# Kernel optimization log

Measured on AMD Instinct MI355X. Metric: run time of the kernel, lower is better.

Reference implementation:

```python
import jax, jax.numpy as jnp
import numpy as np

SR = 2  # sr_ratio

def _avgpool2x2(x):
    # x: [B,C,H,W] -> [B,C,H//2,W//2]
    B, C, H, W = x.shape
    return x.reshape(B, C, H // SR, SR, W // SR, SR).mean(axis=(3, 5))

def setup_inputs() -> dict:
    key = jax.random.key(0)
    ks = jax.random.split(key, 6)
    B, C, H, W = 8, 256, 64, 64
    d = C // 8
    sc_qk = 1.0 / np.sqrt(C)
    return {
        "x": jax.random.normal(ks[0], (B, C, H, W), jnp.float32),
        "wq": jax.random.normal(ks[1], (d, C), jnp.float32) * sc_qk,
        "wk": jax.random.normal(ks[2], (d, C), jnp.float32) * sc_qk,
        "wv": jax.random.normal(ks[3], (C, C), jnp.float32) * sc_qk,
        "wo": jax.random.normal(ks[4], (C, C), jnp.float32) * sc_qk,
        "gamma": jax.random.normal(ks[5], (1,), jnp.float32),
    }

def reference(x, wq, wk, wv, wo, gamma):
    B, C, H, W = x.shape
    N = H * W
    d = wq.shape[0]
    # q: conv1x1 then flatten+transpose -> [B, N, d]
    q = jnp.einsum('dc,bchw->bhwd', wq, x).reshape(B, N, d)
    # spatial reduction of K/V source
    x_kv = _avgpool2x2(x)
    Hk, Wk = x_kv.shape[2], x_kv.shape[3]
    Nk = Hk * Wk
    k = jnp.einsum('dc,bchw->bdhw', wk, x_kv).reshape(B, d, Nk)   # [B,d,Nk]
    v = jnp.einsum('oc,bchw->bohw', wv, x_kv).reshape(B, C, Nk)   # [B,C,Nk]
    # attn = softmax(q @ k / sqrt(d)) over Nk
    attn = jax.nn.softmax(jnp.einsum('bnd,bdm->bnm', q, k) / jnp.sqrt(jnp.float32(d)), axis=-1)
    # out = v @ attn^T -> [B,C,N]
    out = jnp.einsum('bcm,bnm->bcn', v, attn).reshape(B, C, H, W)
    out = jnp.einsum('oc,bchw->bohw', wo, out)
    return x + gamma[0] * out
```

## Files before the change

### kernel.cpp

```cpp
#include <hip/hip_runtime.h>

#define BB 8
#define CC 256
#define NN 4096
#define DD 32
#define NK 1024

typedef unsigned short u16;
typedef unsigned int   u32;
typedef __attribute__((ext_vector_type(8))) short bf16x8;
typedef __attribute__((ext_vector_type(4))) float f32x4;

#define MFMA16 __builtin_amdgcn_mfma_f32_16x16x32_bf16

#define OFF_WVO  0u
#define OFF_WQB  32768u
#define OFF_WKB  36864u
#define OFF_QF   40960u
#define OFF_KF   565248u
#define OFF_VOF  696320u

__device__ __forceinline__ u16 f2bf(float f) {
    u32 u = __float_as_uint(f);
    u += 0x7FFFu + ((u >> 16) & 1u);
    return (u16)(u >> 16);
}

__device__ __forceinline__ u32 cvt_pk_bf16(float lo, float hi) {
    u32 r;
    asm("v_cvt_pk_bf16_f32 %0, %1, %2" : "=v"(r) : "v"(lo), "v"(hi));
    return r;
}

__launch_bounds__(1024)
__global__ void wprep_kernel(const float* __restrict__ wq, const float* __restrict__ wk,
                             const float* __restrict__ wv, const float* __restrict__ wo,
                             u16* __restrict__ wqb, u16* __restrict__ wkb,
                             u16* __restrict__ wvob) {
    __shared__ float part[4][256];
    int o = blockIdx.x, t = threadIdx.x;
    int jq = t >> 8, c = t & 255;
    const float* wvp = wv + (size_t)(jq * 64) * CC + c;
    const float* wop = wo + o * CC + jq * 64;
    float acc = 0.f;
#pragma unroll 8
    for (int i = 0; i < 64; ++i)
        acc += wop[i] * wvp[(size_t)i * CC];
    part[jq][c] = acc;
    __syncthreads();
    if (t < 256)
        wvob[o * CC + t] = f2bf(part[0][t] + part[1][t] + part[2][t] + part[3][t]);
    if (o < 8) {
        const float QS = 0.17677669529663687f * 1.4426950408889634f;
        int id = o * 1024 + t;
        wqb[id] = f2bf(wq[id] * QS);
    } else if (o < 16) {
        int id = (o - 8) * 1024 + t;
        wkb[id] = f2bf(wk[id]);
    }
}

__launch_bounds__(256)
__global__ void proj_kernel(const float* __restrict__ x,
                            const u16* __restrict__ wqb, const u16* __restrict__ wkb,
                            const u16* __restrict__ wvob,
                            u16* __restrict__ qF, u16* __restrict__ kF,
                            u16* __restrict__ voF) {
    int t = threadIdx.x, w = t >> 6, l = t & 63, l15 = l & 15, lg = l >> 4;
    const f32x4 fz = {0.f, 0.f, 0.f, 0.f};

    if (blockIdx.x < 256) {
        __shared__ float xl[64 * 136];
        int b = blockIdx.x & 7, nb = blockIdx.x >> 3;
        int n0 = nb * 128;
        f32x4 acc[2][2];
        acc[0][0] = fz; acc[0][1] = fz; acc[1][0] = fz; acc[1][1] = fz;
        int cr = t >> 2, seg = (t & 3) * 32;
        for (int ch = 0; ch < 4; ++ch) {
            int c0 = ch * 64;
            const float* xs = x + ((size_t)(b * CC + c0 + cr)) * NN + n0 + seg;
#pragma unroll
            for (int p = 0; p < 8; ++p)
                *(float4*)&xl[cr * 136 + seg + p * 4] = *(const float4*)(xs + p * 4);
            __syncthreads();
#pragma unroll
            for (int ks = 0; ks < 2; ++ks) {
                int klo = ks * 32 + lg * 8;
#pragma unroll
                for (int i = 0; i < 2; ++i) {
                    int nl = w * 32 + i * 16 + l15;
                    float f0 = xl[(klo + 0) * 136 + nl];
                    float f1 = xl[(klo + 1) * 136 + nl];
                    float f2 = xl[(klo + 2) * 136 + nl];
                    float f3 = xl[(klo + 3) * 136 + nl];
                    float f4 = xl[(klo + 4) * 136 + nl];
                    float f5 = xl[(klo + 5) * 136 + nl];
                    float f6 = xl[(klo + 6) * 136 + nl];
                    float f7 = xl[(klo + 7) * 136 + nl];
                    union { u32 u[4]; bf16x8 v; } cv;
                    cv.u[0] = cvt_pk_bf16(f0, f1);
                    cv.u[1] = cvt_pk_bf16(f2, f3);
                    cv.u[2] = cvt_pk_bf16(f4, f5);
                    cv.u[3] = cvt_pk_bf16(f6, f7);
#pragma unroll
                    for (int dt = 0; dt < 2; ++dt) {
                        bf16x8 bq = *(const bf16x8*)(wqb + (size_t)(dt * 16 + l15) * CC + c0 + klo);
                        acc[i][dt] = MFMA16(cv.v, bq, acc[i][dt], 0, 0, 0);
                    }
                }
            }
            __syncthreads();
        }
        u16* outp = qF + (size_t)b * 256 * 512;
#pragma unroll
        for (int i = 0; i < 2; ++i)
#pragma unroll
            for (int dt = 0; dt < 2; ++dt)
#pragma unroll
                for (int r2 = 0; r2 < 4; ++r2) {
                    int tile = nb * 8 + w * 2 + i;
                    int dhi = dt * 2 + (l15 >> 3);
                    outp[((size_t)tile * 64 + dhi * 16 + lg * 4 + r2) * 8 + (l15 & 7)]
                        = f2bf(acc[i][dt][r2]);
                }
    } else {
        __shared__ u16 pl[64 * 42];
        int blk2 = blockIdx.x - 256;
        int b = blk2 & 7, hk = blk2 >> 3;
        f32x4 acck = fz;
        f32x4 accv[2][4];
#pragma unroll
        for (int mt = 0; mt < 2; ++mt)
#pragma unroll
            for (int ot = 0; ot < 4; ++ot) accv[mt][ot] = fz;

        int cr = t >> 2, w8 = (t & 3) * 8;
        for (int ch = 0; ch < 4; ++ch) {
            int c0 = ch * 64;
            const float* xs = x + ((size_t)(b * CC + c0 + cr)) * NN + (2 * hk) * 64 + w8 * 2;
            float4 A0 = *(const float4*)(xs +  0), A1 = *(const float4*)(xs +  4);
            float4 A2 = *(const float4*)(xs +  8), A3 = *(const float4*)(xs + 12);
            float4 B0 = *(const float4*)(xs + 64), B1 = *(const float4*)(xs + 68);
            float4 B2 = *(const float4*)(xs + 72), B3 = *(const float4*)(xs + 76);
            float p0 = 0.25f * (A0.x + A0.y + B0.x + B0.y);
            float p1 = 0.25f * (A0.z + A0.w + B0.z + B0.w);
            float p2 = 0.25f * (A1.x + A1.y + B1.x + B1.y);
            float p3 = 0.25f * (A1.z + A1.w + B1.z + B1.w);
            float p4 = 0.25f * (A2.x + A2.y + B2.x + B2.y);
            float p5 = 0.25f * (A2.z + A2.w + B2.z + B2.w);
            float p6 = 0.25f * (A3.x + A3.y + B3.x + B3.y);
            float p7 = 0.25f * (A3.z + A3.w + B3.z + B3.w);
            u32* pw = (u32*)&pl[cr * 42 + w8];
            pw[0] = cvt_pk_bf16(p0, p1);
            pw[1] = cvt_pk_bf16(p2, p3);
            pw[2] = cvt_pk_bf16(p4, p5);
            pw[3] = cvt_pk_bf16(p6, p7);
            __syncthreads();
#pragma unroll
            for (int ks = 0; ks < 2; ++ks) {
                int klo = ks * 32 + lg * 8;
                bf16x8 pm[2];
#pragma unroll
                for (int mt = 0; mt < 2; ++mt) {
                    union { u16 s[8]; bf16x8 v; } cv;
#pragma unroll
                    for (int j = 0; j < 8; ++j)
                        cv.s[j] = pl[(klo + j) * 42 + mt * 16 + l15];
                    pm[mt] = cv.v;
                }
                {
                    bf16x8 bk = *(const bf16x8*)(wkb + (size_t)((w & 1) * 16 + l15) * CC + c0 + klo);
                    acck = MFMA16(pm[w >> 1], bk, acck, 0, 0, 0);
                }
#pragma unroll
                for (int ot = 0; ot < 4; ++ot) {
                    bf16x8 ao = *(const bf16x8*)(wvob + (size_t)(w * 64 + ot * 16 + l15) * CC + c0 + klo);
#pragma unroll
                    for (int mt = 0; mt < 2; ++mt)
                        accv[mt][ot] = MFMA16(ao, pm[mt], accv[mt][ot], 0, 0, 0);
                }
            }
            __syncthreads();
        }
#pragma unroll
        for (int r2 = 0; r2 < 4; ++r2)
            kF[((size_t)(b * 64 + hk * 2 + (w >> 1)) * 64
                + ((w & 1) * 2 + (l15 >> 3)) * 16 + lg * 4 + r2) * 8 + (l15 & 7)]
                = f2bf(acck[r2]);
#pragma unroll
        for (int mt = 0; mt < 2; ++mt)
#pragma unroll
            for (int ot = 0; ot < 4; ++ot)
#pragma unroll
                for (int r2 = 0; r2 < 4; ++r2)
                    voF[(((size_t)(b * 32 + hk) * 16 + w * 4 + ot) * 64
                         + (mt * 2 + (l15 >> 3)) * 16 + lg * 4 + r2) * 8 + (l15 & 7)]
                        = f2bf(accv[mt][ot][r2]);
    }
}

__launch_bounds__(256, 2)
__global__ void attn_kernel(const u16* __restrict__ qF, const u16* __restrict__ kF,
                            const u16* __restrict__ voF, const float* __restrict__ x,
                            const float* __restrict__ gamma, float* __restrict__ out) {
    __shared__ __align__(16) u16   p_lds[2][64 * 40];
    __shared__ __align__(16) float rs_lds[64];

    const int t   = threadIdx.x;
    const int w   = t >> 6, l = t & 63;
    const int l15 = l & 15, lg = l >> 4;
    const int b   = blockIdx.x & 7;
    const int n0  = (blockIdx.x >> 3) << 6;

    bf16x8 qf = *(const bf16x8*)(qF + ((size_t)(b * 256 + (n0 >> 4) + w) * 64 + l) * 8);
    const u16* kfp = kF  + ((size_t)(b * 64) * 64 + l) * 8;
    const u16* vbl = voF + ((size_t)((b * 32) * 16 + w * 4) * 64 + l) * 8;

    u16*       pwp = &p_lds[0][(w * 16 + l15) * 40 + lg * 4];
    const u16* prp = &p_lds[0][l15 * 40 + lg * 8];

    f32x4 acc[4][4];
    const f32x4 fz = {0.f, 0.f, 0.f, 0.f};
#pragma unroll
    for (int j = 0; j < 4; ++j)
#pragma unroll
        for (int of = 0; of < 4; ++of) acc[j][of] = fz;
    float rs = 0.f;

    bf16x8 kf0 = *(const bf16x8*)(kfp);
    bf16x8 kf1 = *(const bf16x8*)(kfp + 512);
    {
        f32x4 c0 = MFMA16(kf0, qf, fz, 0, 0, 0);
        f32x4 c1 = MFMA16(kf1, qf, fz, 0, 0, 0);
        float e0 = __builtin_amdgcn_exp2f(c0[0]);
        float e1 = __builtin_amdgcn_exp2f(c0[1]);
        float e2 = __builtin_amdgcn_exp2f(c0[2]);
        float e3 = __builtin_amdgcn_exp2f(c0[3]);
        float e4 = __builtin_amdgcn_exp2f(c1[0]);
        float e5 = __builtin_amdgcn_exp2f(c1[1]);
        float e6 = __builtin_amdgcn_exp2f(c1[2]);
        float e7 = __builtin_amdgcn_exp2f(c1[3]);
        rs += (e0 + e1 + e2 + e3) + (e4 + e5 + e6 + e7);
        uint2 pw0, pw1;
        pw0.x = cvt_pk_bf16(e0, e1);
        pw0.y = cvt_pk_bf16(e2, e3);
        pw1.x = cvt_pk_bf16(e4, e5);
        pw1.y = cvt_pk_bf16(e6, e7);
        *(uint2*)pwp        = pw0;
        *(uint2*)(pwp + 16) = pw1;
    }
    kf0 = *(const bf16x8*)(kfp + 2 * 512);
    kf1 = *(const bf16x8*)(kfp + 3 * 512);
    bf16x8 vof0[4], vof1[4];
#pragma unroll
    for (int of = 0; of < 4; ++of)
        vof0[of] = *(const bf16x8*)(vbl + of * 512);
#pragma unroll
    for (int of = 0; of < 4; ++of)
        vof1[of] = *(const bf16x8*)(vbl + 8192 + of * 512);
    asm volatile("s_waitcnt lgkmcnt(0)" ::: "memory");
    __builtin_amdgcn_s_barrier();

#pragma unroll 2
    for (int i = 0; i < 31; ++i) {
        const int buf = i & 1;
        const int ip2 = (i + 2 > 31) ? 31 : (i + 2);
        bf16x8 vof2[4];
#pragma unroll
        for (int of = 0; of < 4; ++of)
            vof2[of] = *(const bf16x8*)(vbl + (size_t)ip2 * 8192 + of * 512);
        {
            f32x4 c0 = MFMA16(kf0, qf, fz, 0, 0, 0);
            f32x4 c1 = MFMA16(kf1, qf, fz, 0, 0, 0);
            const int k0i = (2 * i + 4 > 62) ? 62 : (2 * i + 4);
            kf0 = *(const bf16x8*)(kfp + (size_t)k0i * 512);
            kf1 = *(const bf16x8*)(kfp + (size_t)(k0i + 1) * 512);
            float e0 = __builtin_amdgcn_exp2f(c0[0]);
            float e1 = __builtin_amdgcn_exp2f(c0[1]);
            float e2 = __builtin_amdgcn_exp2f(c0[2]);
            float e3 = __builtin_amdgcn_exp2f(c0[3]);
            float e4 = __builtin_amdgcn_exp2f(c1[0]);
            float e5 = __builtin_amdgcn_exp2f(c1[1]);
            float e6 = __builtin_amdgcn_exp2f(c1[2]);
            float e7 = __builtin_amdgcn_exp2f(c1[3]);
            rs += (e0 + e1 + e2 + e3) + (e4 + e5 + e6 + e7);
            uint2 pw0, pw1;
            pw0.x = cvt_pk_bf16(e0, e1);
            pw0.y = cvt_pk_bf16(e2, e3);
            pw1.x = cvt_pk_bf16(e4, e5);
            pw1.y = cvt_pk_bf16(e6, e7);
            u16* pw = pwp + (buf ^ 1) * 2560;
            *(uint2*)pw        = pw0;
            *(uint2*)(pw + 16) = pw1;
        }
        const u16* pr = prp + buf * 2560;
        __builtin_amdgcn_s_setprio(1);
#pragma unroll
        for (int j = 0; j < 4; ++j) {
            bf16x8 pa = *(const bf16x8*)(pr + j * 640);
#pragma unroll
            for (int of = 0; of < 4; ++of)
                acc[j][of] = MFMA16(pa, vof0[of], acc[j][of], 0, 0, 0);
        }
        __builtin_amdgcn_s_setprio(0);
        asm volatile("s_waitcnt lgkmcnt(0)" ::: "memory");
        __builtin_amdgcn_s_barrier();
#pragma unroll
        for (int of = 0; of < 4; ++of) { vof0[of] = vof1[of]; vof1[of] = vof2[of]; }
    }

    {
        const u16* pr = prp + 2560;
#pragma unroll
        for (int j = 0; j < 4; ++j) {
            bf16x8 pa = *(const bf16x8*)(pr + j * 640);
#pragma unroll
            for (int of = 0; of < 4; ++of)
                acc[j][of] = MFMA16(pa, vof0[of], acc[j][of], 0, 0, 0);
        }
    }

    rs += __shfl_xor(rs, 16);
    rs += __shfl_xor(rs, 32);
    if (l < 16) rs_lds[w * 16 + l] = rs;
    __syncthreads();

    float g = gamma[0];
#pragma unroll
    for (int j = 0; j < 4; ++j) {
        int rbase = j * 16 + lg * 4;
        float fa0 = g / rs_lds[rbase + 0];
        float fa1 = g / rs_lds[rbase + 1];
        float fa2 = g / rs_lds[rbase + 2];
        float fa3 = g / rs_lds[rbase + 3];
#pragma unroll
        for (int of = 0; of < 4; ++of) {
            size_t base = ((size_t)(b * CC + w * 64 + of * 16 + l15)) * NN
                        + n0 + j * 16 + lg * 4;
            float4 xv = *(const float4*)(x + base);
            float4 ov;
            ov.x = xv.x + acc[j][of][0] * fa0;
            ov.y = xv.y + acc[j][of][1] * fa1;
            ov.z = xv.z + acc[j][of][2] * fa2;
            ov.w = xv.w + acc[j][of][3] * fa3;
            *(float4*)(out + base) = ov;
        }
    }
}

extern "C" void kernel_launch(void* const* d_in, const int* in_sizes, int n_in,
                              void* d_out, int out_size, void* d_ws, size_t ws_size,
                              hipStream_t stream) {
    const float* x     = (const float*)d_in[0];
    const float* wq    = (const float*)d_in[1];
    const float* wk    = (const float*)d_in[2];
    const float* wv    = (const float*)d_in[3];
    const float* wo    = (const float*)d_in[4];
    const float* gamma = (const float*)d_in[5];
    float* out = (float*)d_out;
    float* ws  = (float*)d_ws;

    u16* wvob = (u16*)(ws + OFF_WVO);
    u16* wqb  = (u16*)(ws + OFF_WQB);
    u16* wkb  = (u16*)(ws + OFF_WKB);
    u16* qF   = (u16*)(ws + OFF_QF);
    u16* kF   = (u16*)(ws + OFF_KF);
    u16* voF  = (u16*)(ws + OFF_VOF);

    wprep_kernel<<<dim3(256), dim3(1024), 0, stream>>>(wq, wk, wv, wo, wqb, wkb, wvob);
    proj_kernel <<<dim3(512), dim3(256),  0, stream>>>(x, wqb, wkb, wvob, qF, kF, voF);
    attn_kernel <<<dim3(512), dim3(256),  0, stream>>>(qF, kF, voF, x, gamma, out);
}
```

Baseline: 57.75 us.

## Merge Q and KV projection blocks to share x tiles via LDS

The Q-projection and KV-projection work for the same two spatial rows now runs in one 512-thread block. Each x chunk is loaded into shared memory once, and four waves compute Q while the other four do the 2x2 average pooling straight from that shared tile before the K/V MFMAs. This roughly halves global reads of x, which was previously read separately by the Q blocks and the KV blocks. It also prefetches the next channel chunk into registers during compute, at the cost of more register pressure, an extra barrier per chunk, and half as many blocks in the grid.

```diff
diff --git a/kernel.cpp b/kernel.cpp
--- a/kernel.cpp
+++ b/kernel.cpp
@@ -60,29 +60,40 @@
     }
 }
 
-__launch_bounds__(256)
+__launch_bounds__(512)
 __global__ void proj_kernel(const float* __restrict__ x,
                             const u16* __restrict__ wqb, const u16* __restrict__ wkb,
                             const u16* __restrict__ wvob,
                             u16* __restrict__ qF, u16* __restrict__ kF,
                             u16* __restrict__ voF) {
+    __shared__ float xl[64 * 136];
+    __shared__ u16 pl[64 * 42];
     int t = threadIdx.x, w = t >> 6, l = t & 63, l15 = l & 15, lg = l >> 4;
+    int b = blockIdx.x & 7, hb = blockIdx.x >> 3;
+    int n0 = hb * 128;
     const f32x4 fz = {0.f, 0.f, 0.f, 0.f};
 
-    if (blockIdx.x < 256) {
-        __shared__ float xl[64 * 136];
-        int b = blockIdx.x & 7, nb = blockIdx.x >> 3;
-        int n0 = nb * 128;
-        f32x4 acc[2][2];
-        acc[0][0] = fz; acc[0][1] = fz; acc[1][0] = fz; acc[1][1] = fz;
-        int cr = t >> 2, seg = (t & 3) * 32;
+    {
+        int cr = t >> 3, sg = (t & 7) * 16;
+        const float* xs = x + ((size_t)(b * CC + cr)) * NN + n0 + sg;
+#pragma unroll
+        for (int p = 0; p < 4; ++p)
+            *(float4*)&xl[cr * 136 + sg + p * 4] = *(const float4*)(xs + p * 4);
+    }
+    __syncthreads();
+
+    if (w < 4) {
+        f32x4 qacc[2][2];
+        qacc[0][0] = fz; qacc[0][1] = fz; qacc[1][0] = fz; qacc[1][1] = fz;
+        int cr = (t & 255) >> 2, seg = (t & 3) * 32;
+        float4 xreg[8];
         for (int ch = 0; ch < 4; ++ch) {
             int c0 = ch * 64;
-            const float* xs = x + ((size_t)(b * CC + c0 + cr)) * NN + n0 + seg;
-#pragma unroll
-            for (int p = 0; p < 8; ++p)
-                *(float4*)&xl[cr * 136 + seg + p * 4] = *(const float4*)(xs + p * 4);
-            __syncthreads();
+            if (ch < 3) {
+                const float* xs = x + ((size_t)(b * CC + c0 + 64 + cr)) * NN + n0 + seg;
+#pragma unroll
+                for (int p = 0; p < 8; ++p) xreg[p] = *(const float4*)(xs + p * 4);
+            }
 #pragma unroll
             for (int ks = 0; ks < 2; ++ks) {
                 int klo = ks * 32 + lg * 8;
@@ -105,11 +116,17 @@
 #pragma unroll
                     for (int dt = 0; dt < 2; ++dt) {
                         bf16x8 bq = *(const bf16x8*)(wqb + (size_t)(dt * 16 + l15) * CC + c0 + klo);
-                        acc[i][dt] = MFMA16(cv.v, bq, acc[i][dt], 0, 0, 0);
+                        qacc[i][dt] = MFMA16(cv.v, bq, qacc[i][dt], 0, 0, 0);
                     }
                 }
             }
             __syncthreads();
+            if (ch < 3) {
+#pragma unroll
+                for (int p = 0; p < 8; ++p)
+                    *(float4*)&xl[cr * 136 + seg + p * 4] = xreg[p];
+            }
+            __syncthreads();
         }
         u16* outp = qF + (size_t)b * 256 * 512;
 #pragma unroll
@@ -118,15 +135,13 @@
             for (int dt = 0; dt < 2; ++dt)
 #pragma unroll
                 for (int r2 = 0; r2 < 4; ++r2) {
-                    int tile = nb * 8 + w * 2 + i;
+                    int tile = hb * 8 + w * 2 + i;
                     int dhi = dt * 2 + (l15 >> 3);
                     outp[((size_t)tile * 64 + dhi * 16 + lg * 4 + r2) * 8 + (l15 & 7)]
-                        = f2bf(acc[i][dt][r2]);
+                        = f2bf(qacc[i][dt][r2]);
                 }
     } else {
-        __shared__ u16 pl[64 * 42];
-        int blk2 = blockIdx.x - 256;
-        int b = blk2 & 7, hk = blk2 >> 3;
+        int w4 = w - 4, t2 = t & 255;
         f32x4 acck = fz;
         f32x4 accv[2][4];
 #pragma unroll
@@ -134,27 +149,22 @@
 #pragma unroll
             for (int ot = 0; ot < 4; ++ot) accv[mt][ot] = fz;
 
-        int cr = t >> 2, w8 = (t & 3) * 8;
+        int cr = t2 >> 2, w8 = (t2 & 3) * 8;
         for (int ch = 0; ch < 4; ++ch) {
             int c0 = ch * 64;
-            const float* xs = x + ((size_t)(b * CC + c0 + cr)) * NN + (2 * hk) * 64 + w8 * 2;
-            float4 A0 = *(const float4*)(xs +  0), A1 = *(const float4*)(xs +  4);
-            float4 A2 = *(const float4*)(xs +  8), A3 = *(const float4*)(xs + 12);
-            float4 B0 = *(const float4*)(xs + 64), B1 = *(const float4*)(xs + 68);
-            float4 B2 = *(const float4*)(xs + 72), B3 = *(const float4*)(xs + 76);
-            float p0 = 0.25f * (A0.x + A0.y + B0.x + B0.y);
-            float p1 = 0.25f * (A0.z + A0.w + B0.z + B0.w);
-            float p2 = 0.25f * (A1.x + A1.y + B1.x + B1.y);
-            float p3 = 0.25f * (A1.z + A1.w + B1.z + B1.w);
-            float p4 = 0.25f * (A2.x + A2.y + B2.x + B2.y);
-            float p5 = 0.25f * (A2.z + A2.w + B2.z + B2.w);
-            float p6 = 0.25f * (A3.x + A3.y + B3.x + B3.y);
-            float p7 = 0.25f * (A3.z + A3.w + B3.z + B3.w);
-            u32* pw = (u32*)&pl[cr * 42 + w8];
-            pw[0] = cvt_pk_bf16(p0, p1);
-            pw[1] = cvt_pk_bf16(p2, p3);
-            pw[2] = cvt_pk_bf16(p4, p5);
-            pw[3] = cvt_pk_bf16(p6, p7);
+            {
+                const float* xr = &xl[cr * 136];
+                u32 pw[4];
+#pragma unroll
+                for (int j = 0; j < 4; ++j) {
+                    int q0 = 2 * (w8 + 2 * j), q1 = 2 * (w8 + 2 * j + 1);
+                    float v0 = 0.25f * (xr[q0] + xr[q0 + 1] + xr[64 + q0] + xr[65 + q0]);
+                    float v1 = 0.25f * (xr[q1] + xr[q1 + 1] + xr[64 + q1] + xr[65 + q1]);
+                    pw[j] = cvt_pk_bf16(v0, v1);
+                }
+                u32* pd = (u32*)&pl[cr * 42 + w8];
+                pd[0] = pw[0]; pd[1] = pw[1]; pd[2] = pw[2]; pd[3] = pw[3];
+            }
             __syncthreads();
 #pragma unroll
             for (int ks = 0; ks < 2; ++ks) {
@@ -169,12 +179,12 @@
                     pm[mt] = cv.v;
                 }
                 {
-                    bf16x8 bk = *(const bf16x8*)(wkb + (size_t)((w & 1) * 16 + l15) * CC + c0 + klo);
-                    acck = MFMA16(pm[w >> 1], bk, acck, 0, 0, 0);
+                    bf16x8 bk = *(const bf16x8*)(wkb + (size_t)((w4 & 1) * 16 + l15) * CC + c0 + klo);
+                    acck = MFMA16(pm[w4 >> 1], bk, acck, 0, 0, 0);
                 }
 #pragma unroll
                 for (int ot = 0; ot < 4; ++ot) {
-                    bf16x8 ao = *(const bf16x8*)(wvob + (size_t)(w * 64 + ot * 16 + l15) * CC + c0 + klo);
+                    bf16x8 ao = *(const bf16x8*)(wvob + (size_t)(w4 * 64 + ot * 16 + l15) * CC + c0 + klo);
 #pragma unroll
                     for (int mt = 0; mt < 2; ++mt)
                         accv[mt][ot] = MFMA16(ao, pm[mt], accv[mt][ot], 0, 0, 0);
@@ -182,10 +192,11 @@
             }
             __syncthreads();
         }
+        int hk = hb;
 #pragma unroll
         for (int r2 = 0; r2 < 4; ++r2)
-            kF[((size_t)(b * 64 + hk * 2 + (w >> 1)) * 64
-                + ((w & 1) * 2 + (l15 >> 3)) * 16 + lg * 4 + r2) * 8 + (l15 & 7)]
+            kF[((size_t)(b * 64 + hk * 2 + (w4 >> 1)) * 64
+                + ((w4 & 1) * 2 + (l15 >> 3)) * 16 + lg * 4 + r2) * 8 + (l15 & 7)]
                 = f2bf(acck[r2]);
 #pragma unroll
         for (int mt = 0; mt < 2; ++mt)
@@ -193,7 +204,7 @@
             for (int ot = 0; ot < 4; ++ot)
 #pragma unroll
                 for (int r2 = 0; r2 < 4; ++r2)
-                    voF[(((size_t)(b * 32 + hk) * 16 + w * 4 + ot) * 64
+                    voF[(((size_t)(b * 32 + hk) * 16 + w4 * 4 + ot) * 64
                          + (mt * 2 + (l15 >> 3)) * 16 + lg * 4 + r2) * 8 + (l15 & 7)]
                         = f2bf(accv[mt][ot][r2]);
     }
@@ -368,6 +379,6 @@
     u16* voF  = (u16*)(ws + OFF_VOF);
 
     wprep_kernel<<<dim3(256), dim3(1024), 0, stream>>>(wq, wk, wv, wo, wqb, wkb, wvob);
-    proj_kernel <<<dim3(512), dim3(256),  0, stream>>>(x, wqb, wkb, wvob, qF, kF, voF);
+    proj_kernel <<<dim3(256), dim3(512),  0, stream>>>(x, wqb, wkb, wvob, qF, kF, voF);
     attn_kernel <<<dim3(512), dim3(256),  0, stream>>>(qF, kF, voF, x, gamma, out);
 }
```

Result: slower. 62.39 us (+8.0%).

## Merge weight prep with Q projection, split KV projection, prefetch pooled x

Applied to the files above, without the earlier changes.

The weight preparation (Wo·Wv product, Wk conversion) now runs in the same launch as the Q projection, and Q reads fp32 Wq directly and converts it to bf16 in registers, so the separate wqb buffer is gone. The K/V projection moves to its own kernel that register-prefetches the next channel chunk of x while computing the current one. This is meant to hide the serial weight-prep launch behind Q-projection work and overlap global loads with MFMA. The trade-offs are a Wo·Wv matvec that is now unsplit (256-long loop per thread), redundant Wq conversion in every block, and more registers used for prefetching.

```diff
diff --git a/kernel.cpp b/kernel.cpp
--- a/kernel.cpp
+++ b/kernel.cpp
@@ -32,171 +32,188 @@
     return r;
 }
 
-__launch_bounds__(1024)
-__global__ void wprep_kernel(const float* __restrict__ wq, const float* __restrict__ wk,
-                             const float* __restrict__ wv, const float* __restrict__ wo,
-                             u16* __restrict__ wqb, u16* __restrict__ wkb,
-                             u16* __restrict__ wvob) {
-    __shared__ float part[4][256];
-    int o = blockIdx.x, t = threadIdx.x;
-    int jq = t >> 8, c = t & 255;
-    const float* wvp = wv + (size_t)(jq * 64) * CC + c;
-    const float* wop = wo + o * CC + jq * 64;
-    float acc = 0.f;
+__launch_bounds__(256)
+__global__ void qwv_kernel(const float* __restrict__ x,  const float* __restrict__ wq,
+                           const float* __restrict__ wk, const float* __restrict__ wv,
+                           const float* __restrict__ wo,
+                           u16* __restrict__ qF, u16* __restrict__ wkb,
+                           u16* __restrict__ wvob) {
+    int t = threadIdx.x;
+    const float QS = 0.17677669529663687f * 1.4426950408889634f;
+
+    if (blockIdx.x >= 256) {
+        int obk = blockIdx.x - 256, c = t;
+        const float* wop = wo + obk * CC;
+        float acc = 0.f;
 #pragma unroll 8
-    for (int i = 0; i < 64; ++i)
-        acc += wop[i] * wvp[(size_t)i * CC];
-    part[jq][c] = acc;
-    __syncthreads();
-    if (t < 256)
-        wvob[o * CC + t] = f2bf(part[0][t] + part[1][t] + part[2][t] + part[3][t]);
-    if (o < 8) {
-        const float QS = 0.17677669529663687f * 1.4426950408889634f;
-        int id = o * 1024 + t;
-        wqb[id] = f2bf(wq[id] * QS);
-    } else if (o < 16) {
-        int id = (o - 8) * 1024 + t;
-        wkb[id] = f2bf(wk[id]);
-    }
+        for (int j = 0; j < CC; ++j)
+            acc += wop[j] * wv[(size_t)j * CC + c];
+        wvob[obk * CC + c] = f2bf(acc);
+        if (obk < DD)
+            wkb[obk * CC + c] = f2bf(wk[obk * CC + c]);
+        return;
+    }
+
+    __shared__ float xl[64 * 136];
+    int w = t >> 6, l = t & 63, l15 = l & 15, lg = l >> 4;
+    int b = blockIdx.x & 7, nb = blockIdx.x >> 3;
+    int n0 = nb * 128;
+    const f32x4 fz = {0.f, 0.f, 0.f, 0.f};
+    f32x4 acc[2][2];
+    acc[0][0] = fz; acc[0][1] = fz; acc[1][0] = fz; acc[1][1] = fz;
+    int cr = t >> 2, seg = (t & 3) * 32;
+    for (int ch = 0; ch < 4; ++ch) {
+        int c0 = ch * 64;
+        const float* xs = x + ((size_t)(b * CC + c0 + cr)) * NN + n0 + seg;
+#pragma unroll
+        for (int p = 0; p < 8; ++p)
+            *(float4*)&xl[cr * 136 + seg + p * 4] = *(const float4*)(xs + p * 4);
+        __syncthreads();
+#pragma unroll
+        for (int ks = 0; ks < 2; ++ks) {
+            int klo = ks * 32 + lg * 8;
+            union { u32 u[4]; bf16x8 v; } bq[2];
+#pragma unroll
+            for (int dt = 0; dt < 2; ++dt) {
+                const float* wqr = wq + (size_t)(dt * 16 + l15) * CC + c0 + klo;
+                float4 a4 = *(const float4*)wqr;
+                float4 b4 = *(const float4*)(wqr + 4);
+                bq[dt].u[0] = cvt_pk_bf16(a4.x * QS, a4.y * QS);
+                bq[dt].u[1] = cvt_pk_bf16(a4.z * QS, a4.w * QS);
+                bq[dt].u[2] = cvt_pk_bf16(b4.x * QS, b4.y * QS);
+                bq[dt].u[3] = cvt_pk_bf16(b4.z * QS, b4.w * QS);
+            }
+#pragma unroll
+            for (int i = 0; i < 2; ++i) {
+                int nl = w * 32 + i * 16 + l15;
+                float f0 = xl[(klo + 0) * 136 + nl];
+                float f1 = xl[(klo + 1) * 136 + nl];
+                float f2 = xl[(klo + 2) * 136 + nl];
+                float f3 = xl[(klo + 3) * 136 + nl];
+                float f4 = xl[(klo + 4) * 136 + nl];
+                float f5 = xl[(klo + 5) * 136 + nl];
+                float f6 = xl[(klo + 6) * 136 + nl];
+                float f7 = xl[(klo + 7) * 136 + nl];
+                union { u32 u[4]; bf16x8 v; } cv;
+                cv.u[0] = cvt_pk_bf16(f0, f1);
+                cv.u[1] = cvt_pk_bf16(f2, f3);
+                cv.u[2] = cvt_pk_bf16(f4, f5);
+                cv.u[3] = cvt_pk_bf16(f6, f7);
+#pragma unroll
+                for (int dt = 0; dt < 2; ++dt)
+                    acc[i][dt] = MFMA16(cv.v, bq[dt].v, acc[i][dt], 0, 0, 0);
+            }
+        }
+        __syncthreads();
+    }
+    u16* outp = qF + (size_t)b * 256 * 512;
+#pragma unroll
+    for (int i = 0; i < 2; ++i)
+#pragma unroll
+        for (int dt = 0; dt < 2; ++dt)
+#pragma unroll
+            for (int r2 = 0; r2 < 4; ++r2) {
+                int tile = nb * 8 + w * 2 + i;
+                int dhi = dt * 2 + (l15 >> 3);
+                outp[((size_t)tile * 64 + dhi * 16 + lg * 4 + r2) * 8 + (l15 & 7)]
+                    = f2bf(acc[i][dt][r2]);
+            }
 }
 
 __launch_bounds__(256)
-__global__ void proj_kernel(const float* __restrict__ x,
-                            const u16* __restrict__ wqb, const u16* __restrict__ wkb,
-                            const u16* __restrict__ wvob,
-                            u16* __restrict__ qF, u16* __restrict__ kF,
-                            u16* __restrict__ voF) {
+__global__ void kv_kernel(const float* __restrict__ x,
+                          const u16* __restrict__ wkb, const u16* __restrict__ wvob,
+                          u16* __restrict__ kF, u16* __restrict__ voF) {
+    __shared__ u16 pl[64 * 42];
     int t = threadIdx.x, w = t >> 6, l = t & 63, l15 = l & 15, lg = l >> 4;
     const f32x4 fz = {0.f, 0.f, 0.f, 0.f};
-
-    if (blockIdx.x < 256) {
-        __shared__ float xl[64 * 136];
-        int b = blockIdx.x & 7, nb = blockIdx.x >> 3;
-        int n0 = nb * 128;
-        f32x4 acc[2][2];
-        acc[0][0] = fz; acc[0][1] = fz; acc[1][0] = fz; acc[1][1] = fz;
-        int cr = t >> 2, seg = (t & 3) * 32;
-        for (int ch = 0; ch < 4; ++ch) {
-            int c0 = ch * 64;
-            const float* xs = x + ((size_t)(b * CC + c0 + cr)) * NN + n0 + seg;
-#pragma unroll
-            for (int p = 0; p < 8; ++p)
-                *(float4*)&xl[cr * 136 + seg + p * 4] = *(const float4*)(xs + p * 4);
-            __syncthreads();
-#pragma unroll
-            for (int ks = 0; ks < 2; ++ks) {
-                int klo = ks * 32 + lg * 8;
-#pragma unroll
-                for (int i = 0; i < 2; ++i) {
-                    int nl = w * 32 + i * 16 + l15;
-                    float f0 = xl[(klo + 0) * 136 + nl];
-                    float f1 = xl[(klo + 1) * 136 + nl];
-                    float f2 = xl[(klo + 2) * 136 + nl];
-                    float f3 = xl[(klo + 3) * 136 + nl];
-                    float f4 = xl[(klo + 4) * 136 + nl];
-                    float f5 = xl[(klo + 5) * 136 + nl];
-                    float f6 = xl[(klo + 6) * 136 + nl];
-                    float f7 = xl[(klo + 7) * 136 + nl];
-                    union { u32 u[4]; bf16x8 v; } cv;
-                    cv.u[0] = cvt_pk_bf16(f0, f1);
-                    cv.u[1] = cvt_pk_bf16(f2, f3);
-                    cv.u[2] = cvt_pk_bf16(f4, f5);
-                    cv.u[3] = cvt_pk_bf16(f6, f7);
-#pragma unroll
-                    for (int dt = 0; dt < 2; ++dt) {
-                        bf16x8 bq = *(const bf16x8*)(wqb + (size_t)(dt * 16 + l15) * CC + c0 + klo);
-                        acc[i][dt] = MFMA16(cv.v, bq, acc[i][dt], 0, 0, 0);
-                    }
-                }
-            }
-            __syncthreads();
-        }
-        u16* outp = qF + (size_t)b * 256 * 512;
-#pragma unroll
-        for (int i = 0; i < 2; ++i)
-#pragma unroll
-            for (int dt = 0; dt < 2; ++dt)
-#pragma unroll
-                for (int r2 = 0; r2 < 4; ++r2) {
-                    int tile = nb * 8 + w * 2 + i;
-                    int dhi = dt * 2 + (l15 >> 3);
-                    outp[((size_t)tile * 64 + dhi * 16 + lg * 4 + r2) * 8 + (l15 & 7)]
-                        = f2bf(acc[i][dt][r2]);
-                }
-    } else {
-        __shared__ u16 pl[64 * 42];
-        int blk2 = blockIdx.x - 256;
-        int b = blk2 & 7, hk = blk2 >> 3;
-        f32x4 acck = fz;
-        f32x4 accv[2][4];
-#pragma unroll
-        for (int mt = 0; mt < 2; ++mt)
-#pragma unroll
-            for (int ot = 0; ot < 4; ++ot) accv[mt][ot] = fz;
-
-        int cr = t >> 2, w8 = (t & 3) * 8;
-        for (int ch = 0; ch < 4; ++ch) {
-            int c0 = ch * 64;
-            const float* xs = x + ((size_t)(b * CC + c0 + cr)) * NN + (2 * hk) * 64 + w8 * 2;
-            float4 A0 = *(const float4*)(xs +  0), A1 = *(const float4*)(xs +  4);
-            float4 A2 = *(const float4*)(xs +  8), A3 = *(const float4*)(xs + 12);
-            float4 B0 = *(const float4*)(xs + 64), B1 = *(const float4*)(xs + 68);
-            float4 B2 = *(const float4*)(xs + 72), B3 = *(const float4*)(xs + 76);
-            float p0 = 0.25f * (A0.x + A0.y + B0.x + B0.y);
-            float p1 = 0.25f * (A0.z + A0.w + B0.z + B0.w);
-            float p2 = 0.25f * (A1.x + A1.y + B1.x + B1.y);
-            float p3 = 0.25f * (A1.z + A1.w + B1.z + B1.w);
-            float p4 = 0.25f * (A2.x + A2.y + B2.x + B2.y);
-            float p5 = 0.25f * (A2.z + A2.w + B2.z + B2.w);
-            float p6 = 0.25f * (A3.x + A3.y + B3.x + B3.y);
-            float p7 = 0.25f * (A3.z + A3.w + B3.z + B3.w);
+    int b = blockIdx.x & 7, hk = blockIdx.x >> 3;
+    f32x4 acck = fz;
+    f32x4 accv[2][4];
+#pragma unroll
+    for (int mt = 0; mt < 2; ++mt)
+#pragma unroll
+        for (int ot = 0; ot < 4; ++ot) accv[mt][ot] = fz;
+
+    int cr = t >> 2, w8 = (t & 3) * 8;
+    const float* xbase = x + ((size_t)(b * CC + cr)) * NN + (2 * hk) * 64 + w8 * 2;
+
+    float4 xr[8], xn[8];
+    {
+        const float* xs = xbase;
+        xr[0] = *(const float4*)(xs +  0); xr[1] = *(const float4*)(xs +  4);
+        xr[2] = *(const float4*)(xs +  8); xr[3] = *(const float4*)(xs + 12);
+        xr[4] = *(const float4*)(xs + 64); xr[5] = *(const float4*)(xs + 68);
+        xr[6] = *(const float4*)(xs + 72); xr[7] = *(const float4*)(xs + 76);
+    }
+
+    for (int ch = 0; ch < 4; ++ch) {
+        int c0 = ch * 64;
+        if (ch < 3) {
+            const float* xs = xbase + (size_t)(c0 + 64) * NN;
+            xn[0] = *(const float4*)(xs +  0); xn[1] = *(const float4*)(xs +  4);
+            xn[2] = *(const float4*)(xs +  8); xn[3] = *(const float4*)(xs + 12);
+            xn[4] = *(const float4*)(xs + 64); xn[5] = *(const float4*)(xs + 68);
+            xn[6] = *(const float4*)(xs + 72); xn[7] = *(const float4*)(xs + 76);
+        }
+        {
+            float p0 = 0.25f * (xr[0].x + xr[0].y + xr[4].x + xr[4].y);
+            float p1 = 0.25f * (xr[0].z + xr[0].w + xr[4].z + xr[4].w);
+            float p2 = 0.25f * (xr[1].x + xr[1].y + xr[5].x + xr[5].y);
+            float p3 = 0.25f * (xr[1].z + xr[1].w + xr[5].z + xr[5].w);
+            float p4 = 0.25f * (xr[2].x + xr[2].y + xr[6].x + xr[6].y);
+            float p5 = 0.25f * (xr[2].z + xr[2].w + xr[6].z + xr[6].w);
+            float p6 = 0.25f * (xr[3].x + xr[3].y + xr[7].x + xr[7].y);
+            float p7 = 0.25f * (xr[3].z + xr[3].w + xr[7].z + xr[7].w);
             u32* pw = (u32*)&pl[cr * 42 + w8];
             pw[0] = cvt_pk_bf16(p0, p1);
             pw[1] = cvt_pk_bf16(p2, p3);
             pw[2] = cvt_pk_bf16(p4, p5);
             pw[3] = cvt_pk_bf16(p6, p7);
-            __syncthreads();
-#pragma unroll
-            for (int ks = 0; ks < 2; ++ks) {
-                int klo = ks * 32 + lg * 8;
-                bf16x8 pm[2];
-#pragma unroll
-                for (int mt = 0; mt < 2; ++mt) {
-                    union { u16 s[8]; bf16x8 v; } cv;
-#pragma unroll
-                    for (int j = 0; j < 8; ++j)
-                        cv.s[j] = pl[(klo + j) * 42 + mt * 16 + l15];
-                    pm[mt] = cv.v;
-                }
-                {
-                    bf16x8 bk = *(const bf16x8*)(wkb + (size_t)((w & 1) * 16 + l15) * CC + c0 + klo);
-                    acck = MFMA16(pm[w >> 1], bk, acck, 0, 0, 0);
-                }
-#pragma unroll
-                for (int ot = 0; ot < 4; ++ot) {
-                    bf16x8 ao = *(const bf16x8*)(wvob + (size_t)(w * 64 + ot * 16 + l15) * CC + c0 + klo);
-#pragma unroll
-                    for (int mt = 0; mt < 2; ++mt)
-                        accv[mt][ot] = MFMA16(ao, pm[mt], accv[mt][ot], 0, 0, 0);
-                }
-            }
-            __syncthreads();
-        }
-#pragma unroll
-        for (int r2 = 0; r2 < 4; ++r2)
-            kF[((size_t)(b * 64 + hk * 2 + (w >> 1)) * 64
-                + ((w & 1) * 2 + (l15 >> 3)) * 16 + lg * 4 + r2) * 8 + (l15 & 7)]
-                = f2bf(acck[r2]);
-#pragma unroll
-        for (int mt = 0; mt < 2; ++mt)
-#pragma unroll
-            for (int ot = 0; ot < 4; ++ot)
-#pragma unroll
-                for (int r2 = 0; r2 < 4; ++r2)
-                    voF[(((size_t)(b * 32 + hk) * 16 + w * 4 + ot) * 64
-                         + (mt * 2 + (l15 >> 3)) * 16 + lg * 4 + r2) * 8 + (l15 & 7)]
-                        = f2bf(accv[mt][ot][r2]);
-    }
+        }
+        __syncthreads();
+#pragma unroll
+        for (int ks = 0; ks < 2; ++ks) {
+            int klo = ks * 32 + lg * 8;
+            bf16x8 pm[2];
+#pragma unroll
+            for (int mt = 0; mt < 2; ++mt) {
+                union { u16 s[8]; bf16x8 v; } cv;
+#pragma unroll
+                for (int j = 0; j < 8; ++j)
+                    cv.s[j] = pl[(klo + j) * 42 + mt * 16 + l15];
+                pm[mt] = cv.v;
+            }
+            {
+                bf16x8 bk = *(const bf16x8*)(wkb + (size_t)((w & 1) * 16 + l15) * CC + c0 + klo);
+                acck = MFMA16(pm[w >> 1], bk, acck, 0, 0, 0);
+            }
+#pragma unroll
+            for (int ot = 0; ot < 4; ++ot) {
+                bf16x8 ao = *(const bf16x8*)(wvob + (size_t)(w * 64 + ot * 16 + l15) * CC + c0 + klo);
+#pragma unroll
+                for (int mt = 0; mt < 2; ++mt)
+                    accv[mt][ot] = MFMA16(ao, pm[mt], accv[mt][ot], 0, 0, 0);
+            }
+        }
+        __syncthreads();
+#pragma unroll
+        for (int p = 0; p < 8; ++p) xr[p] = xn[p];
+    }
+#pragma unroll
+    for (int r2 = 0; r2 < 4; ++r2)
+        kF[((size_t)(b * 64 + hk * 2 + (w >> 1)) * 64
+            + ((w & 1) * 2 + (l15 >> 3)) * 16 + lg * 4 + r2) * 8 + (l15 & 7)]
+            = f2bf(acck[r2]);
+#pragma unroll
+    for (int mt = 0; mt < 2; ++mt)
+#pragma unroll
+        for (int ot = 0; ot < 4; ++ot)
+#pragma unroll
+            for (int r2 = 0; r2 < 4; ++r2)
+                voF[(((size_t)(b * 32 + hk) * 16 + w * 4 + ot) * 64
+                     + (mt * 2 + (l15 >> 3)) * 16 + lg * 4 + r2) * 8 + (l15 & 7)]
+                    = f2bf(accv[mt][ot][r2]);
 }
 
 __launch_bounds__(256, 2)
@@ -361,13 +378,12 @@
     float* ws  = (float*)d_ws;
 
     u16* wvob = (u16*)(ws + OFF_WVO);
-    u16* wqb  = (u16*)(ws + OFF_WQB);
     u16* wkb  = (u16*)(ws + OFF_WKB);
     u16* qF   = (u16*)(ws + OFF_QF);
     u16* kF   = (u16*)(ws + OFF_KF);
     u16* voF  = (u16*)(ws + OFF_VOF);
 
-    wprep_kernel<<<dim3(256), dim3(1024), 0, stream>>>(wq, wk, wv, wo, wqb, wkb, wvob);
-    proj_kernel <<<dim3(512), dim3(256),  0, stream>>>(x, wqb, wkb, wvob, qF, kF, voF);
-    attn_kernel <<<dim3(512), dim3(256),  0, stream>>>(qF, kF, voF, x, gamma, out);
-}
+    qwv_kernel <<<dim3(512), dim3(256), 0, stream>>>(x, wq, wk, wv, wo, qF, wkb, wvob);
+    kv_kernel  <<<dim3(256), dim3(256), 0, stream>>>(x, wkb, wvob, kF, voF);
+    attn_kernel<<<dim3(512), dim3(256), 0, stream>>>(qF, kF, voF, x, gamma, out);
+}
```

Result: slower. 66.97 us (+16.0%).
